# Optimization experiments

Measured on AMD Instinct MI355X. Metric: run time of the kernel, lower is better.

## Reference

```python
import jax, jax.numpy as jnp
import numpy as np

N_HEAD = 16
N_KV_HEAD = 4
D_HEAD = 128
RMS_EPS = 1.1920929e-07  # torch default eps for fp32 rms_norm


def _rms_norm(x):
    return x * jax.lax.rsqrt(jnp.mean(x * x, axis=-1, keepdims=True) + RMS_EPS)


def _rotary_tables(n_pos, dim):
    # dim = d_head; freq table has dim//2 entries (half of them zero)
    angular_freq = (1.0 / 1024.0) ** jnp.linspace(0.0, 1.0, dim // 4, dtype=jnp.float32)
    angular_freq = jnp.concatenate([angular_freq, jnp.zeros(dim // 4, jnp.float32)])
    theta = jnp.arange(n_pos, dtype=jnp.float32)[:, None] * angular_freq[None, :]
    return jnp.cos(theta), jnp.sin(theta)


def _apply_rotary(x):
    # x: (B, H, T, D). Faithful to source: cos/sin indexed by x.shape[-3] (= H),
    # broadcast over the time axis.
    n = x.shape[-3]
    cos, sin = _rotary_tables(n, x.shape[-1])
    cos = cos[None, :, None, :]
    sin = sin[None, :, None, :]
    xf = x.astype(jnp.float32)
    x1, x2 = jnp.split(xf, 2, axis=-1)
    y1 = x1 * cos + x2 * sin
    y2 = -x1 * sin + x2 * cos
    return jnp.concatenate([y1, y2], axis=-1).astype(x.dtype)


def setup_inputs() -> dict:
    key = jax.random.key(0)
    k1, k2, k3, k4 = jax.random.split(key, 4)
    B, T, C = 2, 2048, 2048
    return {
        "x": jax.random.normal(k1, (B, T, C), jnp.float32),
        "Wq": jax.random.normal(k2, (C, C), jnp.float32) * 0.02,
        "Wkv": jax.random.normal(k3, (2 * N_KV_HEAD * D_HEAD, C), jnp.float32) * 0.02,
        "Wproj": jax.random.normal(k4, (C, C), jnp.float32) * 0.02,
        "tok_masks": jnp.ones((B, T), jnp.int32),
    }


def reference(x, Wq, Wkv, Wproj, tok_masks):
    B, T, C = x.shape
    nh, nkv, dh = N_HEAD, N_KV_HEAD, D_HEAD

    q = (x @ Wq.T).reshape(B, T, nh, dh).transpose(0, 2, 1, 3)          # (B,nh,T,dh)
    kv = x @ Wkv.T                                                       # (B,T,2*nkv*dh)
    k, v = jnp.split(kv, 2, axis=2)
    k = k.reshape(B, T, nkv, dh).transpose(0, 2, 1, 3)                   # (B,nkv,T,dh)
    v = v.reshape(B, T, nkv, dh).transpose(0, 2, 1, 3)

    q, k = _rms_norm(q), _rms_norm(k)
    q, k = _apply_rotary(q), _apply_rotary(k)

    # GQA: repeat kv heads to match query heads
    rep = nh // nkv
    k = jnp.repeat(k, rep, axis=1)
    v = jnp.repeat(v, rep, axis=1)

    scale = 1.0 / jnp.sqrt(jnp.float32(dh))
    scores = jnp.einsum("bhqd,bhkd->bhqk", q, k) * scale                 # (B,nh,T,T)
    causal = jnp.tril(jnp.ones((T, T), bool))
    scores = jnp.where(causal[None, None], scores, -jnp.inf)
    attn = jax.nn.softmax(scores, axis=-1)
    y = jnp.einsum("bhqk,bhkd->bhqd", attn, v)                           # (B,nh,T,dh)
    y = y.transpose(0, 2, 1, 3).reshape(B, T, C)
    y = y @ Wproj.T
    return (y, jnp.float32(0.0))
```

## Files before the change

kernel.cpp:

```cpp
#include <hip/hip_runtime.h>
#include <hip/hip_bf16.h>

#define T_SEQ 2048
#define BATCH 2
#define CDIM  2048
#define NH    16
#define NKV   4
#define DH    128

typedef __attribute__((ext_vector_type(8))) short bfrag;
typedef __attribute__((ext_vector_type(4))) float ffrag;
typedef __hip_bfloat16 bf16;

__device__ __forceinline__ void gll16(const bf16* __restrict__ g, bf16* lds) {
    __builtin_amdgcn_global_load_lds((const __attribute__((address_space(1))) void*)g,
                                     (__attribute__((address_space(3))) void*)lds, 16, 0, 0);
}

template<int N> __device__ __forceinline__ void vmw() {
    static_assert(N >= 0 && N <= 6, "vmcnt range");
    if constexpr      (N == 0) asm volatile("s_waitcnt vmcnt(0)" ::: "memory");
    else if constexpr (N == 1) asm volatile("s_waitcnt vmcnt(1)" ::: "memory");
    else if constexpr (N == 2) asm volatile("s_waitcnt vmcnt(2)" ::: "memory");
    else if constexpr (N == 3) asm volatile("s_waitcnt vmcnt(3)" ::: "memory");
    else if constexpr (N == 4) asm volatile("s_waitcnt vmcnt(4)" ::: "memory");
    else if constexpr (N == 5) asm volatile("s_waitcnt vmcnt(5)" ::: "memory");
    else                       asm volatile("s_waitcnt vmcnt(6)" ::: "memory");
}
__device__ __forceinline__ void barx() {
    asm volatile("" ::: "memory");
    __builtin_amdgcn_s_barrier();
    asm volatile("" ::: "memory");
}

constexpr int sv_c(int P, int L, int LPP, int p) {
    return p == P - 1 ? L - 5 : (L - 5) + (p + 1) * (LPP - 1);
}
constexpr int dv_c(int L, int p) { int r = L - 5 - (p + 1); return r < 0 ? 0 : r; }

struct bf16x4 { bf16 a, b, c, d; };
#define N4_X   (BATCH * T_SEQ * CDIM / 4)
#define N4_WQ  (CDIM * CDIM / 4)
#define N4_WKV (2 * NKV * DH * CDIM / 4)
#define N4_WP  (CDIM * CDIM / 4)
__global__ __launch_bounds__(256) void cast_all(
    const float* __restrict__ x, const float* __restrict__ wq,
    const float* __restrict__ wkv, const float* __restrict__ wp,
    bf16* __restrict__ xb, bf16* __restrict__ wqb, bf16* __restrict__ wkvb, bf16* __restrict__ wpb)
{
    int j = blockIdx.x * 256 + threadIdx.x;
    const float* s; bf16* d;
    if (j < N4_X) { s = x; d = xb; }
    else {
        j -= N4_X;
        if (j < N4_WQ) { s = wq; d = wqb; }
        else {
            j -= N4_WQ;
            if (j < N4_WKV) { s = wkv; d = wkvb; }
            else { j -= N4_WKV; if (j >= N4_WP) return; s = wp; d = wpb; }
        }
    }
    float4 f = ((const float4*)s)[j];
    bf16x4 o{__float2bfloat16(f.x), __float2bfloat16(f.y),
             __float2bfloat16(f.z), __float2bfloat16(f.w)};
    ((bf16x4*)d)[j] = o;
}

template<int BM, int MODE>
__device__ __forceinline__ void gemm8_body(
    const bf16* __restrict__ A, const bf16* __restrict__ W, int m0, int n0,
    bf16* __restrict__ out0, bf16* __restrict__ out1, float* __restrict__ outf,
    bf16* __restrict__ sA, bf16* __restrict__ sB)
{
    constexpr int MREP = BM / 32;
    constexpr int P    = MREP / 2;
    constexpr int LA   = BM / 64;
    constexpr int L    = LA + 4;
    constexpr int LPP  = L / P;
    constexpr int NT   = CDIM / 64;
    constexpr int ASZ  = BM * 64;
    constexpr int BSZ  = 256 * 64;

    const int lane = threadIdx.x & 63;
    const int w    = threadIdx.x >> 6;
    const int wm   = w >> 2, wn = w & 3;
    const int lr   = lane & 15, quad = lane >> 4;
    const int srow = lane >> 3;
    const int scol = ((lane & 7) ^ srow) << 3;

    const bf16* Ag[LA];
    const bf16* Bg[4];
    #pragma unroll
    for (int j = 0; j < LA; ++j) Ag[j] = A + (size_t)(m0 + j * 64 + w * 8 + srow) * CDIM + scol;
    #pragma unroll
    for (int j = 0; j < 4; ++j)  Bg[j] = W + (size_t)(n0 + j * 64 + w * 8 + srow) * CDIM + scol;

    ffrag acc[MREP][4] = {};

    #pragma unroll
    for (int j = 0; j < 4; ++j)  gll16(Bg[j], sB + j * 4096 + w * 512);
    #pragma unroll
    for (int j = 0; j < LA; ++j) gll16(Ag[j], sA + j * 4096 + w * 512);
    vmw<L - 5>();
    barx();

    for (int t = 0; t < NT; ++t) {
        const int cur = t & 1;
        const bool last = (t == NT - 1);
        const int knext = (t + 1) * 64;
        bf16* sAc = sA + cur * ASZ;
        bf16* sBc = sB + cur * BSZ;
        bf16* sAn = sA + (cur ^ 1) * ASZ;
        bf16* sBn = sB + (cur ^ 1) * BSZ;
        bfrag bgr[2][4];

#define PHASE(pp)                                                                          \
        {                                                                                  \
            if (pp == 0) {                                                                 \
                _Pragma("unroll")                                                          \
                for (int g = 0; g < 4; ++g) {                                              \
                    const int br = (wn * 64 + g * 16 + lr) * 64;                           \
                    bgr[0][g] = *(const bfrag*)&sBc[br + ((quad ^ (lr & 7)) << 3)];        \
                    bgr[1][g] = *(const bfrag*)&sBc[br + (((4 | quad) ^ (lr & 7)) << 3)];  \
                }                                                                          \
            }                                                                              \
            bfrag af0[2], af1[2];                                                          \
            _Pragma("unroll")                                                              \
            for (int f2 = 0; f2 < 2; ++f2) {                                               \
                const int ar = ((2 * pp + f2) * 32 + wm * 16 + lr) * 64;                   \
                af0[f2] = *(const bfrag*)&sAc[ar + ((quad ^ (lr & 7)) << 3)];              \
                af1[f2] = *(const bfrag*)&sAc[ar + (((4 | quad) ^ (lr & 7)) << 3)];        \
            }                                                                              \
            if (!last) {                                                                   \
                _Pragma("unroll")                                                          \
                for (int l = pp * LPP; l < (pp + 1) * LPP; ++l) {                          \
                    if (l < 4) gll16(Bg[l] + knext, sBn + l * 4096 + w * 512);             \
                    else       gll16(Ag[l - 4] + knext, sAn + (l - 4) * 4096 + w * 512);   \
                }                                                                          \
            }                                                                              \
            barx();                                                                        \
            __builtin_amdgcn_s_setprio(1);                                                 \
            _Pragma("unroll")                                                              \
            for (int f2 = 0; f2 < 2; ++f2)                                                 \
                _Pragma("unroll")                                                          \
                for (int g = 0; g < 4; ++g) {                                              \
                    acc[2 * pp + f2][g] = __builtin_amdgcn_mfma_f32_16x16x32_bf16(         \
                        af0[f2], bgr[0][g], acc[2 * pp + f2][g], 0, 0, 0);                 \
                    acc[2 * pp + f2][g] = __builtin_amdgcn_mfma_f32_16x16x32_bf16(         \
                        af1[f2], bgr[1][g], acc[2 * pp + f2][g], 0, 0, 0);                 \
                }                                                                          \
            __builtin_amdgcn_s_setprio(0);                                                 \
            if (!last) vmw<sv_c(P, L, LPP, pp)>();                                         \
            else if (pp != P - 1) vmw<dv_c(L, pp)>();                                      \
            barx();                                                                        \
        }

        PHASE(0)
        PHASE(1)
        if constexpr (P == 4) {
            PHASE(2)
            PHASE(3)
        }
#undef PHASE
    }

    #pragma unroll
    for (int f = 0; f < MREP; ++f) {
        #pragma unroll
        for (int g = 0; g < 4; ++g) {
            #pragma unroll
            for (int i = 0; i < 4; ++i) {
                const int m = m0 + f * 32 + wm * 16 + quad * 4 + i;
                const int n = n0 + wn * 64 + g * 16 + lr;
                const float v = acc[f][g][i];
                if constexpr (MODE == 0) {
                    int b = m >> 11, tt = m & (T_SEQ - 1);
                    int h = n >> 7, d = n & (DH - 1);
                    out0[(((size_t)(b * NH + h) * T_SEQ + tt) << 7) + d] = __float2bfloat16(v);
                } else if constexpr (MODE == 1) {
                    int b = m >> 11, tt = m & (T_SEQ - 1);
                    if (n < NKV * DH) {
                        int h = n >> 7, d = n & (DH - 1);
                        out0[(((size_t)(b * NKV + h) * T_SEQ + tt) << 7) + d] = __float2bfloat16(v);
                    } else {
                        int n2 = n - NKV * DH;
                        int h = n2 >> 7, d = n2 & (DH - 1);
                        out1[(((size_t)(b * NKV + h) * DH + d) << 11) + tt] = __float2bfloat16(v);
                    }
                } else {
                    outf[(size_t)m * CDIM + n] = v;
                }
            }
        }
    }
}

__global__ __launch_bounds__(512, 2) void gemm_qkv(
    const bf16* __restrict__ A, const bf16* __restrict__ Wq, const bf16* __restrict__ Wkv,
    bf16* __restrict__ q, bf16* __restrict__ k, bf16* __restrict__ vt)
{
    __shared__ __align__(16) bf16 sA[2 * 256 * 64];
    __shared__ __align__(16) bf16 sB[2 * 256 * 64];
    const int bid = blockIdx.x;
    const int sb = (bid & 7) * 24 + (bid >> 3);
    const int mt = sb & 15, nt = sb >> 4;
    if (nt < 8) gemm8_body<256, 0>(A, Wq,  mt * 256, nt * 256,       q, nullptr, nullptr, sA, sB);
    else        gemm8_body<256, 1>(A, Wkv, mt * 256, (nt - 8) * 256, k, vt,      nullptr, sA, sB);
}

__global__ __launch_bounds__(512, 2) void gemm_proj(
    const bf16* __restrict__ A, const bf16* __restrict__ W, float* __restrict__ outf)
{
    __shared__ __align__(16) bf16 sA[2 * 128 * 64];
    __shared__ __align__(16) bf16 sB[2 * 256 * 64];
    const int bid = blockIdx.x;
    const int sb = (bid & 7) * 32 + (bid >> 3);
    const int mt = sb & 31, nt = sb >> 5;
    gemm8_body<128, 2>(A, W, mt * 128, nt * 256, nullptr, nullptr, outf, sA, sB);
    if (blockIdx.x == 0 && threadIdx.x == 0)
        outf[(size_t)BATCH * T_SEQ * CDIM] = 0.0f;
}

#define QROWS (BATCH * NH * T_SEQ)
#define KROWS (BATCH * NKV * T_SEQ)
__global__ __launch_bounds__(256) void normrope_k(bf16* __restrict__ qb, bf16* __restrict__ kb) {
    int row = blockIdx.x * 4 + (threadIdx.x >> 6);
    bf16* bufb; int nheads;
    if (row < QROWS) { bufb = qb; nheads = NH; }
    else { row -= QROWS; bufb = kb; nheads = NKV; }
    const int h = (row >> 11) % nheads;
    bf16* p = bufb + (size_t)row * DH;
    const int d = threadIdx.x & 63;
    float x1 = __bfloat162float(p[d]);
    float x2 = __bfloat162float(p[d + 64]);
    float ss = x1 * x1 + x2 * x2;
    #pragma unroll
    for (int off = 32; off; off >>= 1) ss += __shfl_xor(ss, off);
    float r = rsqrtf(ss * (1.0f / 128.0f) + 1.1920929e-07f);
    x1 *= r; x2 *= r;
    float freq = (d < 32) ? exp2f(-10.0f * (float)d * (1.0f / 31.0f)) : 0.0f;
    float th = (float)h * freq;
    float c, s;
    __sincosf(th, &s, &c);
    p[d]      = __float2bfloat16(x1 * c + x2 * s);
    p[d + 64] = __float2bfloat16(-x1 * s + x2 * c);
}

__global__ __launch_bounds__(512, 2) void attn_k(const bf16* __restrict__ Q, const bf16* __restrict__ K,
                                                 const bf16* __restrict__ VT, bf16* __restrict__ Y)
{
    const int lane = threadIdx.x & 63;
    const int w = threadIdx.x >> 6;
    const int g = w >> 2, wl = w & 3;
    const int p = blockIdx.x, h = blockIdx.y, b = blockIdx.z;
    const int lr = lane & 15, quad = lane >> 4, lk = quad * 8;
    const bf16* Qb = Q  + (size_t)(b * NH  + h)        * T_SEQ * DH;
    const bf16* Kb = K  + (size_t)(b * NKV + (h >> 2)) * T_SEQ * DH;
    const bf16* Vb = VT + (size_t)(b * NKV + (h >> 2)) * DH * T_SEQ;

    __shared__ __align__(16) union ShmU {
        struct { bf16 SK[2][32 * 128]; bf16 SV[2][128 * 32]; bf16 SP[8][2][16 * 32]; } s;
        ffrag MRG[9 * 4 * 64];
    } shm;
    bf16* SKg = shm.s.SK[g];
    bf16* SVg = shm.s.SV[g];

    const int k_r0 = wl * 8 + (lane >> 4);
    const int k_ch = lane & 15;
    const int v_r0 = wl * 32 + (lane >> 2);
    const int v_ch = lane & 3;
    const int vsw = (lr + (lr >> 2)) & 3;
    const int prow_r = ((lr & 3) << 2) | (lr >> 2);
    const int psw = (prow_r + (prow_r >> 2)) & 3;
    const float scale = 0.08838834764831845f;

    for (int pass = 0; pass < 2; ++pass) {
        const int qb = pass ? (15 - p) : p;
        const int nc = 2 * (qb + 1);
        const int q0 = qb * 128 + wl * 32;

        bfrag qf[2][4];
        #pragma unroll
        for (int t = 0; t < 2; ++t)
            #pragma unroll
            for (int dc = 0; dc < 4; ++dc)
                qf[t][dc] = *(const bfrag*)(Qb + (size_t)(q0 + t * 16 + lr) * DH + dc * 32 + lk);

        float lp[2][4] = {};
        ffrag o[2][8] = {};

        bfrag kr[2], vr[2];
        {
            const int b0 = g * 32;
            #pragma unroll
            for (int j = 0; j < 2; ++j) {
                kr[j] = *(const bfrag*)(Kb + (size_t)(b0 + k_r0 + j * 4) * DH + k_ch * 8);
                vr[j] = *(const bfrag*)(Vb + (size_t)(v_r0 + j * 16) * T_SEQ + b0 + v_ch * 8);
            }
        }

        for (int c = 0; c < nc; ++c) {
            const int base = c * 64 + g * 32;
            __syncthreads();
            #pragma unroll
            for (int j = 0; j < 2; ++j) {
                int krow = k_r0 + j * 4;
                *(bfrag*)&SKg[krow * 128 + ((k_ch ^ (krow & 15))) * 8] = kr[j];
                int vrow = v_r0 + j * 16;
                *(bfrag*)&SVg[vrow * 32 + ((v_ch ^ ((vrow + (vrow >> 2)) & 3))) * 8] = vr[j];
            }
            if (c + 1 < nc) {
                const int nb = base + 64;
                #pragma unroll
                for (int j = 0; j < 2; ++j) {
                    kr[j] = *(const bfrag*)(Kb + (size_t)(nb + k_r0 + j * 4) * DH + k_ch * 8);
                    vr[j] = *(const bfrag*)(Vb + (size_t)(v_r0 + j * 16) * T_SEQ + nb + v_ch * 8);
                }
            }
            __syncthreads();

            ffrag s2[2][2] = {};
            #pragma unroll
            for (int kt = 0; kt < 2; ++kt)
                #pragma unroll
                for (int dc = 0; dc < 4; ++dc) {
                    bfrag kf = *(const bfrag*)&SKg[(kt * 16 + lr) * 128 + (((dc << 2) | quad) ^ lr) * 8];
                    s2[0][kt] = __builtin_amdgcn_mfma_f32_16x16x32_bf16(qf[0][dc], kf, s2[0][kt], 0, 0, 0);
                    s2[1][kt] = __builtin_amdgcn_mfma_f32_16x16x32_bf16(qf[1][dc], kf, s2[1][kt], 0, 0, 0);
                }

            const bool maskc = (c >= 2 * qb);
            #pragma unroll
            for (int t = 0; t < 2; ++t)
                #pragma unroll
                for (int kt = 0; kt < 2; ++kt) {
                    const int col = base + kt * 16 + lr;
                    #pragma unroll
                    for (int i = 0; i < 4; ++i) {
                        const int row = q0 + t * 16 + quad * 4 + i;
                        float e = (!maskc || col <= row) ? __expf(fmaf(s2[t][kt][i], scale, -16.0f)) : 0.0f;
                        lp[t][i] += e;
                        const int pr = i * 4 + quad;
                        const int pc = (kt * 2 + (lr >> 3)) ^ ((quad + i) & 3);
                        shm.s.SP[w][t][pr * 32 + pc * 8 + (lr & 7)] = __float2bfloat16(e);
                    }
                }

            bfrag pf0 = *(const bfrag*)&shm.s.SP[w][0][prow_r * 32 + ((quad ^ psw)) * 8];
            bfrag pf1 = *(const bfrag*)&shm.s.SP[w][1][prow_r * 32 + ((quad ^ psw)) * 8];
            #pragma unroll
            for (int dt = 0; dt < 8; ++dt) {
                bfrag vf = *(const bfrag*)&SVg[(dt * 16 + lr) * 32 + ((quad ^ vsw)) * 8];
                o[0][dt] = __builtin_amdgcn_mfma_f32_16x16x32_bf16(pf0, vf, o[0][dt], 0, 0, 0);
                o[1][dt] = __builtin_amdgcn_mfma_f32_16x16x32_bf16(pf1, vf, o[1][dt], 0, 0, 0);
            }
        }

        __syncthreads();
        #pragma unroll
        for (int t = 0; t < 2; ++t) {
            if (g == 1) {
                #pragma unroll
                for (int d = 0; d < 8; ++d) shm.MRG[(d * 4 + wl) * 64 + lane] = o[t][d];
                ffrag l4 = {lp[t][0], lp[t][1], lp[t][2], lp[t][3]};
                shm.MRG[(8 * 4 + wl) * 64 + lane] = l4;
            }
            __syncthreads();
            if (g == 0) {
                #pragma unroll
                for (int d = 0; d < 8; ++d) o[t][d] += shm.MRG[(d * 4 + wl) * 64 + lane];
                ffrag l4 = shm.MRG[(8 * 4 + wl) * 64 + lane];
                float inv[4];
                #pragma unroll
                for (int i = 0; i < 4; ++i) {
                    float l = lp[t][i] + l4[i];
                    #pragma unroll
                    for (int off = 1; off < 16; off <<= 1) l += __shfl_xor(l, off);
                    inv[i] = 1.0f / l;
                }
                #pragma unroll
                for (int dt = 0; dt < 8; ++dt)
                    #pragma unroll
                    for (int i = 0; i < 4; ++i) {
                        int row = q0 + t * 16 + quad * 4 + i;
                        Y[((size_t)(b * T_SEQ) + row) * CDIM + h * DH + dt * 16 + lr] =
                            __float2bfloat16(o[t][dt][i] * inv[i]);
                    }
            }
            __syncthreads();
        }
    }
}

extern "C" void kernel_launch(void* const* d_in, const int* in_sizes, int n_in,
                              void* d_out, int out_size, void* d_ws, size_t ws_size,
                              hipStream_t stream) {
    const float* x     = (const float*)d_in[0];
    const float* Wq    = (const float*)d_in[1];
    const float* Wkv   = (const float*)d_in[2];
    const float* Wproj = (const float*)d_in[3];
    float* out = (float*)d_out;

    char* ws = (char*)d_ws;
    size_t off = 0;
    auto alloc = [&](size_t bytes) { void* p = ws + off; off += (bytes + 255) & ~255ULL; return p; };
    bf16* xb   = (bf16*)alloc((size_t)BATCH * T_SEQ * CDIM * 2);
    bf16* wqb  = (bf16*)alloc((size_t)CDIM * CDIM * 2);
    bf16* wkvb = (bf16*)alloc((size_t)2 * NKV * DH * CDIM * 2);
    bf16* wpb  = (bf16*)alloc((size_t)CDIM * CDIM * 2);
    bf16* qb   = (bf16*)alloc((size_t)BATCH * NH * T_SEQ * DH * 2);
    bf16* kb   = (bf16*)alloc((size_t)BATCH * NKV * T_SEQ * DH * 2);
    bf16* vtb  = (bf16*)alloc((size_t)BATCH * NKV * DH * T_SEQ * 2);
    bf16* y1   = (bf16*)alloc((size_t)BATCH * T_SEQ * CDIM * 2);

    const int total4 = N4_X + N4_WQ + N4_WKV + N4_WP;
    cast_all<<<(total4 + 255) / 256, 256, 0, stream>>>(x, Wq, Wkv, Wproj, xb, wqb, wkvb, wpb);

    gemm_qkv<<<dim3(192), 512, 0, stream>>>(xb, wqb, wkvb, qb, kb, vtb);
    normrope_k<<<(QROWS + KROWS) / 4, 256, 0, stream>>>(qb, kb);
    attn_k<<<dim3(8, NH, BATCH), 512, 0, stream>>>(qb, kb, vtb, y1);
    gemm_proj<<<dim3(256), 512, 0, stream>>>(y1, wpb, out);
}
```

Measured before the change: 305.7 us.

## Restructure GEMM mainloop to BK=32 with 4-buffer, 3-deep prefetch pipeline

The shared GEMM body used by the QKV and output projections goes from a double-buffered BK=64 loop with phased loads to a BK=32 loop. The new loop keeps four LDS stages and issues global-to-LDS loads three tiles ahead, with one barrier per k-step. This needs a new swizzled smem layout and fragment addressing, plus a wider vmcnt wait helper. The aim is to hide global-load latency better, at the cost of twice as many iterations and barriers, each doing half the MFMA work.

```diff
diff --git a/kernel.cpp b/kernel.cpp
--- a/kernel.cpp
+++ b/kernel.cpp
@@ -18,25 +18,26 @@
 }
 
 template<int N> __device__ __forceinline__ void vmw() {
-    static_assert(N >= 0 && N <= 6, "vmcnt range");
-    if constexpr      (N == 0) asm volatile("s_waitcnt vmcnt(0)" ::: "memory");
-    else if constexpr (N == 1) asm volatile("s_waitcnt vmcnt(1)" ::: "memory");
-    else if constexpr (N == 2) asm volatile("s_waitcnt vmcnt(2)" ::: "memory");
-    else if constexpr (N == 3) asm volatile("s_waitcnt vmcnt(3)" ::: "memory");
-    else if constexpr (N == 4) asm volatile("s_waitcnt vmcnt(4)" ::: "memory");
-    else if constexpr (N == 5) asm volatile("s_waitcnt vmcnt(5)" ::: "memory");
-    else                       asm volatile("s_waitcnt vmcnt(6)" ::: "memory");
+    static_assert(N >= 0 && N <= 12, "vmcnt range");
+    if constexpr      (N == 0)  asm volatile("s_waitcnt vmcnt(0)"  ::: "memory");
+    else if constexpr (N == 1)  asm volatile("s_waitcnt vmcnt(1)"  ::: "memory");
+    else if constexpr (N == 2)  asm volatile("s_waitcnt vmcnt(2)"  ::: "memory");
+    else if constexpr (N == 3)  asm volatile("s_waitcnt vmcnt(3)"  ::: "memory");
+    else if constexpr (N == 4)  asm volatile("s_waitcnt vmcnt(4)"  ::: "memory");
+    else if constexpr (N == 5)  asm volatile("s_waitcnt vmcnt(5)"  ::: "memory");
+    else if constexpr (N == 6)  asm volatile("s_waitcnt vmcnt(6)"  ::: "memory");
+    else if constexpr (N == 7)  asm volatile("s_waitcnt vmcnt(7)"  ::: "memory");
+    else if constexpr (N == 8)  asm volatile("s_waitcnt vmcnt(8)"  ::: "memory");
+    else if constexpr (N == 9)  asm volatile("s_waitcnt vmcnt(9)"  ::: "memory");
+    else if constexpr (N == 10) asm volatile("s_waitcnt vmcnt(10)" ::: "memory");
+    else if constexpr (N == 11) asm volatile("s_waitcnt vmcnt(11)" ::: "memory");
+    else                        asm volatile("s_waitcnt vmcnt(12)" ::: "memory");
 }
 __device__ __forceinline__ void barx() {
     asm volatile("" ::: "memory");
     __builtin_amdgcn_s_barrier();
     asm volatile("" ::: "memory");
 }
-
-constexpr int sv_c(int P, int L, int LPP, int p) {
-    return p == P - 1 ? L - 5 : (L - 5) + (p + 1) * (LPP - 1);
-}
-constexpr int dv_c(int L, int p) { int r = L - 5 - (p + 1); return r < 0 ? 0 : r; }
 
 struct bf16x4 { bf16 a, b, c, d; };
 #define N4_X   (BATCH * T_SEQ * CDIM / 4)
@@ -67,102 +68,87 @@
 }
 
 template<int BM, int MODE>
-__device__ __forceinline__ void gemm8_body(
+__device__ __forceinline__ void gemm32_body(
     const bf16* __restrict__ A, const bf16* __restrict__ W, int m0, int n0,
     bf16* __restrict__ out0, bf16* __restrict__ out1, float* __restrict__ outf,
     bf16* __restrict__ sA, bf16* __restrict__ sB)
 {
-    constexpr int MREP = BM / 32;
-    constexpr int P    = MREP / 2;
-    constexpr int LA   = BM / 64;
-    constexpr int L    = LA + 4;
-    constexpr int LPP  = L / P;
-    constexpr int NT   = CDIM / 64;
-    constexpr int ASZ  = BM * 64;
-    constexpr int BSZ  = 256 * 64;
-
-    const int lane = threadIdx.x & 63;
-    const int w    = threadIdx.x >> 6;
+    constexpr int MREP  = BM / 32;
+    constexpr int LA    = BM / 128;
+    constexpr int L     = LA + 2;
+    constexpr int NT    = CDIM / 32;
+    constexpr int DEPTH = 3;
+    constexpr int ASZ   = BM * 32;
+    constexpr int BSZ   = 256 * 32;
+
+    const int tid  = threadIdx.x;
+    const int lane = tid & 63;
+    const int w    = tid >> 6;
     const int wm   = w >> 2, wn = w & 3;
     const int lr   = lane & 15, quad = lane >> 4;
-    const int srow = lane >> 3;
-    const int scol = ((lane & 7) ^ srow) << 3;
-
-    const bf16* Ag[LA];
-    const bf16* Bg[4];
+
+    const int prow_s = tid >> 3;
+    const int ls     = (tid & 7) ^ (prow_s & 7);
+    const int r_s    = 2 * (prow_s & 63) + (ls >> 2);
+    const int k0_s   = (ls & 3) * 8;
+    const int wbase  = w * 512;
+
+    const bf16* Asrc[LA];
+    const bf16* Bsrc[2];
     #pragma unroll
-    for (int j = 0; j < LA; ++j) Ag[j] = A + (size_t)(m0 + j * 64 + w * 8 + srow) * CDIM + scol;
+    for (int j = 0; j < LA; ++j) Asrc[j] = A + (size_t)(m0 + j * 128 + r_s) * CDIM + k0_s;
     #pragma unroll
-    for (int j = 0; j < 4; ++j)  Bg[j] = W + (size_t)(n0 + j * 64 + w * 8 + srow) * CDIM + scol;
+    for (int j = 0; j < 2; ++j)  Bsrc[j] = W + (size_t)(n0 + j * 128 + r_s) * CDIM + k0_s;
+
+    const int soff = ((((lr & 1) << 2) | quad) ^ ((lr >> 1) & 7)) << 3;
 
     ffrag acc[MREP][4] = {};
 
     #pragma unroll
-    for (int j = 0; j < 4; ++j)  gll16(Bg[j], sB + j * 4096 + w * 512);
-    #pragma unroll
-    for (int j = 0; j < LA; ++j) gll16(Ag[j], sA + j * 4096 + w * 512);
-    vmw<L - 5>();
-    barx();
-
-    for (int t = 0; t < NT; ++t) {
-        const int cur = t & 1;
-        const bool last = (t == NT - 1);
-        const int knext = (t + 1) * 64;
-        bf16* sAc = sA + cur * ASZ;
-        bf16* sBc = sB + cur * BSZ;
-        bf16* sAn = sA + (cur ^ 1) * ASZ;
-        bf16* sBn = sB + (cur ^ 1) * BSZ;
-        bfrag bgr[2][4];
-
-#define PHASE(pp)                                                                          \
-        {                                                                                  \
-            if (pp == 0) {                                                                 \
-                _Pragma("unroll")                                                          \
-                for (int g = 0; g < 4; ++g) {                                              \
-                    const int br = (wn * 64 + g * 16 + lr) * 64;                           \
-                    bgr[0][g] = *(const bfrag*)&sBc[br + ((quad ^ (lr & 7)) << 3)];        \
-                    bgr[1][g] = *(const bfrag*)&sBc[br + (((4 | quad) ^ (lr & 7)) << 3)];  \
-                }                                                                          \
-            }                                                                              \
-            bfrag af0[2], af1[2];                                                          \
+    for (int tt = 0; tt < DEPTH; ++tt) {
+        #pragma unroll
+        for (int j = 0; j < 2; ++j)  gll16(Bsrc[j] + tt * 32, sB + tt * BSZ + j * 4096 + wbase);
+        #pragma unroll
+        for (int j = 0; j < LA; ++j) gll16(Asrc[j] + tt * 32, sA + tt * ASZ + j * 4096 + wbase);
+    }
+
+#define GITER(tt, WAITN, PFF)                                                              \
+    {                                                                                      \
+        vmw<WAITN>();                                                                      \
+        barx();                                                                            \
+        const int cur = (tt) & 3;                                                          \
+        bfrag af[MREP], bg[4];                                                             \
+        _Pragma("unroll")                                                                  \
+        for (int f = 0; f < MREP; ++f)                                                     \
+            af[f] = *(const bfrag*)&sA[cur * ASZ + ((f * 16 + wm * 8 + (lr >> 1)) << 6) + soff]; \
+        _Pragma("unroll")                                                                  \
+        for (int g = 0; g < 4; ++g)                                                        \
+            bg[g] = *(const bfrag*)&sB[cur * BSZ + ((wn * 32 + g * 8 + (lr >> 1)) << 6) + soff]; \
+        if (PFF) {                                                                         \
+            const int pb = ((tt) + DEPTH) & 3;                                             \
+            const size_t ko = (size_t)((tt) + DEPTH) * 32;                                 \
             _Pragma("unroll")                                                              \
-            for (int f2 = 0; f2 < 2; ++f2) {                                               \
-                const int ar = ((2 * pp + f2) * 32 + wm * 16 + lr) * 64;                   \
-                af0[f2] = *(const bfrag*)&sAc[ar + ((quad ^ (lr & 7)) << 3)];              \
-                af1[f2] = *(const bfrag*)&sAc[ar + (((4 | quad) ^ (lr & 7)) << 3)];        \
-            }                                                                              \
-            if (!last) {                                                                   \
-                _Pragma("unroll")                                                          \
-                for (int l = pp * LPP; l < (pp + 1) * LPP; ++l) {                          \
-                    if (l < 4) gll16(Bg[l] + knext, sBn + l * 4096 + w * 512);             \
-                    else       gll16(Ag[l - 4] + knext, sAn + (l - 4) * 4096 + w * 512);   \
-                }                                                                          \
-            }                                                                              \
-            barx();                                                                        \
-            __builtin_amdgcn_s_setprio(1);                                                 \
+            for (int j = 0; j < 2; ++j)                                                    \
+                gll16(Bsrc[j] + ko, sB + pb * BSZ + j * 4096 + wbase);                     \
             _Pragma("unroll")                                                              \
-            for (int f2 = 0; f2 < 2; ++f2)                                                 \
-                _Pragma("unroll")                                                          \
-                for (int g = 0; g < 4; ++g) {                                              \
-                    acc[2 * pp + f2][g] = __builtin_amdgcn_mfma_f32_16x16x32_bf16(         \
-                        af0[f2], bgr[0][g], acc[2 * pp + f2][g], 0, 0, 0);                 \
-                    acc[2 * pp + f2][g] = __builtin_amdgcn_mfma_f32_16x16x32_bf16(         \
-                        af1[f2], bgr[1][g], acc[2 * pp + f2][g], 0, 0, 0);                 \
-                }                                                                          \
-            __builtin_amdgcn_s_setprio(0);                                                 \
-            if (!last) vmw<sv_c(P, L, LPP, pp)>();                                         \
-            else if (pp != P - 1) vmw<dv_c(L, pp)>();                                      \
-            barx();                                                                        \
-        }
-
-        PHASE(0)
-        PHASE(1)
-        if constexpr (P == 4) {
-            PHASE(2)
-            PHASE(3)
-        }
-#undef PHASE
+            for (int j = 0; j < LA; ++j)                                                   \
+                gll16(Asrc[j] + ko, sA + pb * ASZ + j * 4096 + wbase);                     \
+        }                                                                                  \
+        __builtin_amdgcn_s_setprio(1);                                                     \
+        _Pragma("unroll")                                                                  \
+        for (int f = 0; f < MREP; ++f)                                                     \
+            _Pragma("unroll")                                                              \
+            for (int g = 0; g < 4; ++g)                                                    \
+                acc[f][g] = __builtin_amdgcn_mfma_f32_16x16x32_bf16(af[f], bg[g], acc[f][g], 0, 0, 0); \
+        __builtin_amdgcn_s_setprio(0);                                                     \
     }
+
+    int t = 0;
+    for (; t < NT - DEPTH; ++t) GITER(t, 2 * L, true)
+    GITER(t, 2 * L, false) ++t;
+    GITER(t, L, false)     ++t;
+    GITER(t, 0, false)
+#undef GITER
 
     #pragma unroll
     for (int f = 0; f < MREP; ++f) {
@@ -174,18 +160,18 @@
                 const int n = n0 + wn * 64 + g * 16 + lr;
                 const float v = acc[f][g][i];
                 if constexpr (MODE == 0) {
-                    int b = m >> 11, tt = m & (T_SEQ - 1);
+                    int b = m >> 11, tt2 = m & (T_SEQ - 1);
                     int h = n >> 7, d = n & (DH - 1);
-                    out0[(((size_t)(b * NH + h) * T_SEQ + tt) << 7) + d] = __float2bfloat16(v);
+                    out0[(((size_t)(b * NH + h) * T_SEQ + tt2) << 7) + d] = __float2bfloat16(v);
                 } else if constexpr (MODE == 1) {
-                    int b = m >> 11, tt = m & (T_SEQ - 1);
+                    int b = m >> 11, tt2 = m & (T_SEQ - 1);
                     if (n < NKV * DH) {
                         int h = n >> 7, d = n & (DH - 1);
-                        out0[(((size_t)(b * NKV + h) * T_SEQ + tt) << 7) + d] = __float2bfloat16(v);
+                        out0[(((size_t)(b * NKV + h) * T_SEQ + tt2) << 7) + d] = __float2bfloat16(v);
                     } else {
                         int n2 = n - NKV * DH;
                         int h = n2 >> 7, d = n2 & (DH - 1);
-                        out1[(((size_t)(b * NKV + h) * DH + d) << 11) + tt] = __float2bfloat16(v);
+                        out1[(((size_t)(b * NKV + h) * DH + d) << 11) + tt2] = __float2bfloat16(v);
                     }
                 } else {
                     outf[(size_t)m * CDIM + n] = v;
@@ -199,24 +185,24 @@
     const bf16* __restrict__ A, const bf16* __restrict__ Wq, const bf16* __restrict__ Wkv,
     bf16* __restrict__ q, bf16* __restrict__ k, bf16* __restrict__ vt)
 {
-    __shared__ __align__(16) bf16 sA[2 * 256 * 64];
-    __shared__ __align__(16) bf16 sB[2 * 256 * 64];
+    __shared__ __align__(16) bf16 sA[4 * 256 * 32];
+    __shared__ __align__(16) bf16 sB[4 * 256 * 32];
     const int bid = blockIdx.x;
     const int sb = (bid & 7) * 24 + (bid >> 3);
     const int mt = sb & 15, nt = sb >> 4;
-    if (nt < 8) gemm8_body<256, 0>(A, Wq,  mt * 256, nt * 256,       q, nullptr, nullptr, sA, sB);
-    else        gemm8_body<256, 1>(A, Wkv, mt * 256, (nt - 8) * 256, k, vt,      nullptr, sA, sB);
+    if (nt < 8) gemm32_body<256, 0>(A, Wq,  mt * 256, nt * 256,       q, nullptr, nullptr, sA, sB);
+    else        gemm32_body<256, 1>(A, Wkv, mt * 256, (nt - 8) * 256, k, vt,      nullptr, sA, sB);
 }
 
 __global__ __launch_bounds__(512, 2) void gemm_proj(
     const bf16* __restrict__ A, const bf16* __restrict__ W, float* __restrict__ outf)
 {
-    __shared__ __align__(16) bf16 sA[2 * 128 * 64];
-    __shared__ __align__(16) bf16 sB[2 * 256 * 64];
+    __shared__ __align__(16) bf16 sA[4 * 128 * 32];
+    __shared__ __align__(16) bf16 sB[4 * 256 * 32];
     const int bid = blockIdx.x;
     const int sb = (bid & 7) * 32 + (bid >> 3);
     const int mt = sb & 31, nt = sb >> 5;
-    gemm8_body<128, 2>(A, W, mt * 128, nt * 256, nullptr, nullptr, outf, sA, sB);
+    gemm32_body<128, 2>(A, W, mt * 128, nt * 256, nullptr, nullptr, outf, sA, sB);
     if (blockIdx.x == 0 && threadIdx.x == 0)
         outf[(size_t)BATCH * T_SEQ * CDIM] = 0.0f;
 }
```

Result: no change. 303.2 us (-0.8%).
